# Optimization experiments

Measured on AMD Instinct MI355X. Metric: run time of the kernel, lower is better.

## Reference

```python
import jax, jax.numpy as jnp
import numpy as np

DECAY = 0.99
EPS = 1e-5
COMMIT_COST = 0.25
VQ_COST = 1.0
COUNTER = 1  # first EMA step (hidden buffers are zero-initialized)


def setup_inputs() -> dict:
    key = jax.random.key(0)
    k1, k2 = jax.random.split(key)
    B, D, T, K = 64, 128, 2048, 1024
    x = jax.random.normal(k1, (B, D, T), dtype=jnp.float32)
    # xavier_uniform for [K, D]
    limit = float(np.sqrt(6.0 / (K + D)))
    embeddings = jax.random.uniform(k2, (K, D), minval=-limit, maxval=limit, dtype=jnp.float32)
    ema_dw_hidden = jnp.zeros((K, D), dtype=jnp.float32)
    ema_cluster_hidden = jnp.zeros((K,), dtype=jnp.float32)
    return {"x": x, "embeddings": embeddings,
            "ema_dw_hidden": ema_dw_hidden, "ema_cluster_hidden": ema_cluster_hidden}


def reference(x, embeddings, ema_dw_hidden, ema_cluster_hidden):
    K, D = embeddings.shape
    xt = jnp.transpose(x, (0, 2, 1))          # [B, T, D]
    flat = xt.reshape(-1, D)                  # [N, D]
    dist = (jnp.sum(flat * flat, axis=1, keepdims=True)
            + jnp.sum(embeddings * embeddings, axis=1)
            - 2.0 * flat @ embeddings.T)      # [N, K]
    idx = jnp.argmin(dist, axis=1)            # [N]
    quantized = embeddings[idx].reshape(xt.shape)  # [B, T, D]

    # --- EMA codebook update (no grad; pure stats) ---
    counts = jax.ops.segment_sum(jnp.ones_like(idx, dtype=jnp.float32), idx, num_segments=K)  # [K]
    hid_cs = ema_cluster_hidden - (ema_cluster_hidden - counts) * (1.0 - DECAY)
    avg_cs = hid_cs / (1.0 - DECAY ** COUNTER)
    n = jnp.sum(avg_cs)
    cs = (avg_cs + EPS) / (n + K * EPS) * n   # Laplace-smoothed cluster size
    dw = jax.ops.segment_sum(flat, idx, num_segments=K)  # [K, D] == encodings.T @ flat
    hid_dw = ema_dw_hidden - (ema_dw_hidden - dw) * (1.0 - DECAY)
    avg_dw = hid_dw / (1.0 - DECAY ** COUNTER)
    new_embeddings = avg_dw / cs[:, None]

    # --- losses + straight-through estimator ---
    sg = jax.lax.stop_gradient
    loss_commit = COMMIT_COST * jnp.mean((xt - sg(quantized)) ** 2)
    loss_vq = VQ_COST * jnp.mean((sg(xt) - quantized) ** 2)
    q_st = xt + sg(quantized - xt)
    out = jnp.transpose(q_st, (0, 2, 1))      # [B, D, T]
    return (out, loss_commit, loss_vq, idx, new_embeddings)
```

## Files before the change

### kernel.cpp

```cpp
#include <hip/hip_runtime.h>

#define NB 64
#define ND 128
#define NT 2048
#define NK 1024
#define NN (NB*NT)
#define DTSTRIDE (ND*NT)

typedef __attribute__((ext_vector_type(8))) short bf16x8;
typedef __attribute__((ext_vector_type(4))) float floatx4;

#define WS_ET    0
#define WS_SSX   131072
#define WS_SSE   262144
#define WS_DW    263168
#define WS_CS    394240
#define WS_CNT   395264
#define WS_IDX   396288
#define WS_LOSS  527360
#define WS_OFFS  527364
#define WS_CUR   528388
#define WS_LIST  529412
#define WS_XT    660736
#define WS_EB    17437952

#define O_OUT 0
#define O_LC  16777216
#define O_LV  16777217
#define O_IDX 16777218
#define O_NE  16908290

#define GLL16(g, l) __builtin_amdgcn_global_load_lds( \
    (const __attribute__((address_space(1))) unsigned int*)(g), \
    (__attribute__((address_space(3))) unsigned int*)(l), 16, 0, 0)

__device__ inline void split1(float v, unsigned short &a, unsigned short &b,
                              unsigned short &c) {
    unsigned int u = __float_as_uint(v);
    a = (unsigned short)(u >> 16);
    float f1 = __uint_as_float(u & 0xffff0000u);
    float r = v - f1;
    unsigned int ur = __float_as_uint(r);
    b = (unsigned short)(ur >> 16);
    float f2 = __uint_as_float(ur & 0xffff0000u);
    float r2 = r - f2;
    c = (unsigned short)(__float_as_uint(r2) >> 16);
}

__device__ inline void split2(float va, float vb, unsigned int &p1,
                              unsigned int &p2, unsigned int &p3) {
    unsigned int ua = __float_as_uint(va), ub = __float_as_uint(vb);
    p1 = (ua >> 16) | (ub & 0xffff0000u);
    float fa = __uint_as_float(ua & 0xffff0000u);
    float fb = __uint_as_float(ub & 0xffff0000u);
    float ra = va - fa, rb = vb - fb;
    unsigned int ura = __float_as_uint(ra), urb = __float_as_uint(rb);
    p2 = (ura >> 16) | (urb & 0xffff0000u);
    float f2a = __uint_as_float(ura & 0xffff0000u);
    float f2b = __uint_as_float(urb & 0xffff0000u);
    float r2a = ra - f2a, r2b = rb - f2b;
    p3 = (__float_as_uint(r2a) >> 16) | (__float_as_uint(r2b) & 0xffff0000u);
}

__global__ void prep_e(const float* __restrict__ emb, float* __restrict__ ET,
                       float* __restrict__ sse, unsigned short* __restrict__ eb1,
                       unsigned short* __restrict__ eb2, unsigned short* __restrict__ eb3) {
    int tid = threadIdx.x;
    int k   = blockIdx.x * 16 + (tid >> 4);
    int l   = tid & 15;
    float ss = 0.f;
    #pragma unroll
    for (int it = 0; it < 2; ++it) {
        int d0 = l * 4 + it * 64;
        float4 v = *(const float4*)(emb + k * ND + d0);
        ET[(d0+0)*NK + k] = v.x;
        ET[(d0+1)*NK + k] = v.y;
        ET[(d0+2)*NK + k] = v.z;
        ET[(d0+3)*NK + k] = v.w;
        ss = fmaf(v.x, v.x, ss); ss = fmaf(v.y, v.y, ss);
        ss = fmaf(v.z, v.z, ss); ss = fmaf(v.w, v.w, ss);
        int dc  = (l >> 3) + it * 2;
        int d5  = d0 & 31;
        int qb  = (d5 >> 3) & 3;
        int sl  = qb ^ ((k >> 1) & 3);
        int off = (dc * NK + k) * 32 + (sl << 3) + (d5 & 7);
        ushort4 a, b, c;
        split1(v.x, a.x, b.x, c.x);
        split1(v.y, a.y, b.y, c.y);
        split1(v.z, a.z, b.z, c.z);
        split1(v.w, a.w, b.w, c.w);
        *(ushort4*)(eb1 + off) = a;
        *(ushort4*)(eb2 + off) = b;
        *(ushort4*)(eb3 + off) = c;
    }
    for (int m = 1; m <= 8; m <<= 1) ss += __shfl_xor(ss, m);
    if (l == 0) sse[k] = ss;
}

__global__ void transpose_x(const float* __restrict__ x, float* __restrict__ xt,
                            float* __restrict__ ssx) {
    __shared__ float tile[128][33];
    int tid = threadIdx.x;
    int b   = blockIdx.x >> 6;
    int t0  = (blockIdx.x & 63) << 5;
    int tl  = tid & 31;
    int dg  = tid >> 5;
    const float* xp = x + b * DTSTRIDE + t0 + tl;
    #pragma unroll
    for (int p = 0; p < 16; ++p) {
        int d = p * 8 + dg;
        tile[d][tl] = xp[d * NT];
    }
    __syncthreads();
    float* xtp = xt + (size_t)(b * NT + t0) * ND;
    #pragma unroll
    for (int c = 0; c < 4; ++c) {
        int d = c * 32 + (tid & 31);
        #pragma unroll
        for (int p = 0; p < 4; ++p) {
            int tr = p * 8 + (tid >> 5);
            xtp[tr * ND + d] = tile[d][tr];
        }
    }
    if (tid < 32) {
        float ss = 0.f;
        #pragma unroll 8
        for (int d = 0; d < ND; ++d) {
            float v = tile[d][tid];
            ss = fmaf(v, v, ss);
        }
        ssx[b * NT + t0 + tid] = ss;
    }
}

__device__ __forceinline__ void stage_eb(int ktp, int dcp, int bufidx, int w, int lane,
        unsigned short* smem, const unsigned short* eb1,
        const unsigned short* eb2, const unsigned short* eb3) {
    int goff = (dcp << 15) + (ktp << 12);
    int bufo = bufidx * 12288;
    #pragma unroll
    for (int i = 0; i < 2; ++i) {
        int ch = (w << 1) + i;
        int so = goff + (ch << 9) + (lane << 3);
        GLL16(eb1 + so, &smem[bufo + 0*4096 + (ch << 9)]);
        GLL16(eb2 + so, &smem[bufo + 1*4096 + (ch << 9)]);
        GLL16(eb3 + so, &smem[bufo + 2*4096 + (ch << 9)]);
    }
}

__device__ __forceinline__ int m3(int v) { return v >= 3 ? v - 3 : v; }

__launch_bounds__(256, 2)
__global__ void gemm_argmin_mfma(const float* __restrict__ xt,
                                 const unsigned short* __restrict__ eb1,
                                 const unsigned short* __restrict__ eb2,
                                 const unsigned short* __restrict__ eb3,
                                 const float* __restrict__ ssx, const float* __restrict__ sse,
                                 const float* __restrict__ x, const float* __restrict__ ET,
                                 float* __restrict__ out, int* __restrict__ idxi,
                                 int* __restrict__ counts, float* __restrict__ loss) {
    __shared__ unsigned short smem[38912];
    int tid = threadIdx.x;
    int b   = blockIdx.x >> 4;
    int t0  = (blockIdx.x & 15) << 7;
    int n0  = b * NT + t0;

    int lane = tid & 63;
    int w    = tid >> 6;
    int c    = lane & 15;
    int q    = lane >> 4;
    int slot = q ^ ((c >> 1) & 3);

    stage_eb(0, 0, 0, w, lane, smem, eb1, eb2, eb3);

    float* ssef = (float*)&smem[36864];
    ((float4*)ssef)[tid] = ((const float4*)sse)[tid];

    bf16x8 af[4][2][3];
    #pragma unroll
    for (int dc = 0; dc < 4; ++dc) {
        #pragma unroll
        for (int i = 0; i < 2; ++i) {
            const float* xp = xt + (size_t)(n0 + w*32 + i*16 + c) * ND + dc*32 + q*8;
            float4 v0 = *(const float4*)(xp + 0);
            float4 v1 = *(const float4*)(xp + 4);
            unsigned int p1[4], p2[4], p3[4];
            split2(v0.x, v0.y, p1[0], p2[0], p3[0]);
            split2(v0.z, v0.w, p1[1], p2[1], p3[1]);
            split2(v1.x, v1.y, p1[2], p2[2], p3[2]);
            split2(v1.z, v1.w, p1[3], p2[3], p3[3]);
            uint4 u;
            u = make_uint4(p1[0], p1[1], p1[2], p1[3]); af[dc][i][0] = *(bf16x8*)&u;
            u = make_uint4(p2[0], p2[1], p2[2], p2[3]); af[dc][i][1] = *(bf16x8*)&u;
            u = make_uint4(p3[0], p3[1], p3[2], p3[3]); af[dc][i][2] = *(bf16x8*)&u;
        }
    }

    float ssxv[8];
    #pragma unroll
    for (int i = 0; i < 2; ++i)
        #pragma unroll
        for (int rr = 0; rr < 4; ++rr)
            ssxv[i*4+rr] = ssx[n0 + w*32 + i*16 + q*4 + rr];

    stage_eb(0, 1, 1, w, lane, smem, eb1, eb2, eb3);

    float bestD[8]; int bestK[8];
    #pragma unroll
    for (int i = 0; i < 8; ++i) { bestD[i] = 3.4e38f; bestK[i] = 0; }

    floatx4 acc[2][8];
    int b3 = 0;

    for (int kt = 0; kt < 8; ++kt) {
        #pragma unroll
        for (int i = 0; i < 2; ++i)
            #pragma unroll
            for (int j = 0; j < 8; ++j)
                acc[i][j] = (floatx4){0.f, 0.f, 0.f, 0.f};

        #pragma unroll
        for (int dc = 0; dc < 4; ++dc) {
            int cur = (dc == 0 || dc == 3) ? b3 : m3(b3 + dc);

            if (kt == 7 && dc == 3) {
                asm volatile("s_waitcnt vmcnt(0) lgkmcnt(0)" ::: "memory");
            } else {
                asm volatile("s_waitcnt vmcnt(6) lgkmcnt(0)" ::: "memory");
            }
            __builtin_amdgcn_s_barrier();

            if (dc == 0) {
                stage_eb(kt, 2, m3(b3 + 2), w, lane, smem, eb1, eb2, eb3);
            } else if (dc == 1) {
                stage_eb(kt, 3, b3, w, lane, smem, eb1, eb2, eb3);
            } else if (dc == 2) {
                if (kt < 7) stage_eb(kt + 1, 0, m3(b3 + 1), w, lane, smem, eb1, eb2, eb3);
            } else {
                if (kt < 7) stage_eb(kt + 1, 1, m3(b3 + 2), w, lane, smem, eb1, eb2, eb3);
            }

            int bufo = cur * 12288;
            __builtin_amdgcn_s_setprio(1);
            #pragma unroll
            for (int j = 0; j < 8; ++j) {
                int ro = bufo + ((j << 4) + c) * 32 + slot * 8;
                bf16x8 b1 = *(const bf16x8*)(&smem[ro + 0*4096]);
                bf16x8 b2 = *(const bf16x8*)(&smem[ro + 1*4096]);
                bf16x8 b3f = *(const bf16x8*)(&smem[ro + 2*4096]);
                #pragma unroll
                for (int i = 0; i < 2; ++i) {
                    acc[i][j] = __builtin_amdgcn_mfma_f32_16x16x32_bf16(af[dc][i][0], b1, acc[i][j], 0, 0, 0);
                    acc[i][j] = __builtin_amdgcn_mfma_f32_16x16x32_bf16(af[dc][i][0], b2, acc[i][j], 0, 0, 0);
                    acc[i][j] = __builtin_amdgcn_mfma_f32_16x16x32_bf16(af[dc][i][1], b1, acc[i][j], 0, 0, 0);
                    acc[i][j] = __builtin_amdgcn_mfma_f32_16x16x32_bf16(af[dc][i][1], b2, acc[i][j], 0, 0, 0);
                    acc[i][j] = __builtin_amdgcn_mfma_f32_16x16x32_bf16(af[dc][i][0], b3f, acc[i][j], 0, 0, 0);
                    acc[i][j] = __builtin_amdgcn_mfma_f32_16x16x32_bf16(af[dc][i][2], b1, acc[i][j], 0, 0, 0);
                }
            }
            __builtin_amdgcn_s_setprio(0);
        }

        #pragma unroll
        for (int j = 0; j < 8; ++j) {
            int   kidx = (kt << 7) + (j << 4) + c;
            float se = ssef[(kt << 7) + (j << 4) + c];
            #pragma unroll
            for (int i = 0; i < 2; ++i) {
                #pragma unroll
                for (int rr = 0; rr < 4; ++rr) {
                    float t1   = ssxv[i*4+rr] + se;
                    float dist = fmaf(-2.f, acc[i][j][rr], t1);
                    if (dist < bestD[i*4+rr]) { bestD[i*4+rr] = dist; bestK[i*4+rr] = kidx; }
                }
            }
        }
        b3 = m3(b3 + 1);
    }

    #pragma unroll
    for (int i = 0; i < 8; ++i) {
        float d = bestD[i]; int kk = bestK[i];
        for (int m = 1; m <= 8; m <<= 1) {
            float od = __shfl_xor(d, m);
            int   ok = __shfl_xor(kk, m);
            if (od < d || (od == d && ok < kk)) { d = od; kk = ok; }
        }
        bestD[i] = d; bestK[i] = kk;
    }
    int* ksh = (int*)smem;
    if (c == 0) {
        float ls = 0.f;
        #pragma unroll
        for (int i = 0; i < 2; ++i)
            #pragma unroll
            for (int rr = 0; rr < 4; ++rr) {
                int r  = w*32 + i*16 + q*4 + rr;
                int n  = n0 + r;
                int kk = bestK[i*4+rr];
                out[O_IDX + n] = (float)kk;
                idxi[n] = kk;
                ksh[r] = kk;
                atomicAdd(&counts[kk], 1);
                ls += bestD[i*4+rr];
            }
        atomicAdd(loss, ls);
    }
    __syncthreads();

    int tl2 = tid & 127;
    int dh  = tid >> 7;
    int kk2 = ksh[tl2];
    const float* xp2 = x + b * DTSTRIDE + t0 + tl2;
    float*       op2 = out + O_OUT + b * DTSTRIDE + t0 + tl2;
    #pragma unroll 4
    for (int s = 0; s < 64; ++s) {
        int d = s * 2 + dh;
        float xv = xp2[d * NT];
        float qv = ET[d * NK + kk2];
        op2[d * NT] = xv + (qv - xv);
    }
}

__global__ void scan_cs(const int* __restrict__ counts, int* __restrict__ offs,
                        int* __restrict__ cur, const float* __restrict__ ch,
                        const float* __restrict__ loss, float* __restrict__ csv,
                        float* __restrict__ out) {
    __shared__ int   s[256];
    __shared__ float red[256];
    int tid = threadIdx.x;
    int c[4]; int sum = 0;
    #pragma unroll
    for (int j = 0; j < 4; ++j) { c[j] = counts[tid*4+j]; sum += c[j]; }
    s[tid] = sum; __syncthreads();
    for (int off = 1; off < 256; off <<= 1) {
        int v = (tid >= off) ? s[tid - off] : 0;
        __syncthreads();
        s[tid] += v;
        __syncthreads();
    }
    int base = (tid == 0) ? 0 : s[tid-1];
    #pragma unroll
    for (int j = 0; j < 4; ++j) {
        offs[tid*4+j] = base; cur[tid*4+j] = base; base += c[j];
    }
    __syncthreads();
    const float DECF = (float)(1.0 - 0.99);
    float sf = 0.f;
    #pragma unroll
    for (int rr = 0; rr < 4; ++rr) {
        int k = tid + rr * 256;
        float cc = (float)counts[k];
        float e = ch[k];
        float hid = e - (e - cc) * DECF;
        sf += hid / DECF;
    }
    red[tid] = sf; __syncthreads();
    for (int off = 128; off > 0; off >>= 1) {
        if (tid < off) red[tid] += red[tid + off];
        __syncthreads();
    }
    float n = red[0];
    const float KEPSF = (float)(1024.0 * 1e-5);
    #pragma unroll
    for (int rr = 0; rr < 4; ++rr) {
        int k = tid + rr * 256;
        float cc = (float)counts[k];
        float e = ch[k];
        float hid = e - (e - cc) * DECF;
        float a = hid / DECF;
        csv[k] = (a + 1e-5f) / (n + KEPSF) * n;
    }
    if (tid == 0) {
        float mean = loss[0] / 16777216.f;
        out[O_LC] = 0.25f * mean;
        out[O_LV] = mean;
    }
}

__global__ void fill_list(const int* __restrict__ idxi, int* __restrict__ cur,
                          int* __restrict__ list) {
    int n = blockIdx.x * 256 + threadIdx.x;
    int k = idxi[n];
    int pos = atomicAdd(&cur[k], 1);
    list[pos] = n;
}

__global__ void dw_sum(const float* __restrict__ xt,
                       const int* __restrict__ counts, const int* __restrict__ offs,
                       const int* __restrict__ list, const float* __restrict__ dwh,
                       const float* __restrict__ csv, float* __restrict__ out) {
    __shared__ float red[128];
    int k = blockIdx.x;
    int d = threadIdx.x & 127;
    int h = threadIdx.x >> 7;
    int cnt = counts[k], base = offs[k];
    float acc = 0.f;
    for (int m = h; m < cnt; m += 2) {
        int n = list[base + m];
        acc += xt[(size_t)n * ND + d];
    }
    if (h == 1) red[d] = acc;
    __syncthreads();
    if (h == 0) {
        const float DECF = (float)(1.0 - 0.99);
        float dwv = acc + red[d];
        int   kd  = k * ND + d;
        float e   = dwh[kd];
        float hid = e - (e - dwv) * DECF;
        float a   = hid / DECF;
        out[O_NE + kd] = a / csv[k];
    }
}

extern "C" void kernel_launch(void* const* d_in, const int* in_sizes, int n_in,
                              void* d_out, int out_size, void* d_ws, size_t ws_size,
                              hipStream_t stream) {
    const float* x   = (const float*)d_in[0];
    const float* emb = (const float*)d_in[1];
    const float* dwh = (const float*)d_in[2];
    const float* ch  = (const float*)d_in[3];
    float* out = (float*)d_out;
    float* ws  = (float*)d_ws;

    float* ET   = ws + WS_ET;
    float* ssx  = ws + WS_SSX;
    float* sse  = ws + WS_SSE;
    float* csv  = ws + WS_CS;
    int*   counts = (int*)(ws + WS_CNT);
    int*   idxi   = (int*)(ws + WS_IDX);
    float* loss   = ws + WS_LOSS;
    int*   offs   = (int*)(ws + WS_OFFS);
    int*   cur    = (int*)(ws + WS_CUR);
    int*   list   = (int*)(ws + WS_LIST);
    float* xt     = ws + WS_XT;
    unsigned short* eb1 = (unsigned short*)(ws + WS_EB);
    unsigned short* eb2 = eb1 + NK * ND;
    unsigned short* eb3 = eb2 + NK * ND;

    hipMemsetAsync(counts, 0, NK * sizeof(int), stream);
    hipMemsetAsync(loss, 0, sizeof(float), stream);

    prep_e         <<<64,   256, 0, stream>>>(emb, ET, sse, eb1, eb2, eb3);
    transpose_x    <<<4096, 256, 0, stream>>>(x, xt, ssx);
    gemm_argmin_mfma<<<1024,256, 0, stream>>>(xt, eb1, eb2, eb3, ssx, sse, x, ET,
                                              out, idxi, counts, loss);
    scan_cs        <<<1,    256, 0, stream>>>(counts, offs, cur, ch, loss, csv, out);
    fill_list      <<<512,  256, 0, stream>>>(idxi, cur, list);
    dw_sum         <<<1024, 256, 0, stream>>>(xt, counts, offs, list, dwh, csv, out);
}
```

Measured before the change: 424.4 us.

## Fuse x transpose and row-norm computation into the GEMM-argmin kernel

Removes the separate transpose_x kernel. The GEMM kernel now loads its 128-token tile of x directly in [D,T] layout, transposes it through shared memory, builds the split-bf16 A fragments and row squared norms from it, and still writes xt for the later dw_sum kernel. This cuts one launch and the extra global read of xt by the GEMM. In exchange it adds shared-memory staging with extra barriers, and the eb staging now starts after the x prologue instead of overlapping with it.

```diff
diff --git a/kernel.cpp b/kernel.cpp
--- a/kernel.cpp
+++ b/kernel.cpp
@@ -97,42 +97,6 @@
     if (l == 0) sse[k] = ss;
 }
 
-__global__ void transpose_x(const float* __restrict__ x, float* __restrict__ xt,
-                            float* __restrict__ ssx) {
-    __shared__ float tile[128][33];
-    int tid = threadIdx.x;
-    int b   = blockIdx.x >> 6;
-    int t0  = (blockIdx.x & 63) << 5;
-    int tl  = tid & 31;
-    int dg  = tid >> 5;
-    const float* xp = x + b * DTSTRIDE + t0 + tl;
-    #pragma unroll
-    for (int p = 0; p < 16; ++p) {
-        int d = p * 8 + dg;
-        tile[d][tl] = xp[d * NT];
-    }
-    __syncthreads();
-    float* xtp = xt + (size_t)(b * NT + t0) * ND;
-    #pragma unroll
-    for (int c = 0; c < 4; ++c) {
-        int d = c * 32 + (tid & 31);
-        #pragma unroll
-        for (int p = 0; p < 4; ++p) {
-            int tr = p * 8 + (tid >> 5);
-            xtp[tr * ND + d] = tile[d][tr];
-        }
-    }
-    if (tid < 32) {
-        float ss = 0.f;
-        #pragma unroll 8
-        for (int d = 0; d < ND; ++d) {
-            float v = tile[d][tid];
-            ss = fmaf(v, v, ss);
-        }
-        ssx[b * NT + t0 + tid] = ss;
-    }
-}
-
 __device__ __forceinline__ void stage_eb(int ktp, int dcp, int bufidx, int w, int lane,
         unsigned short* smem, const unsigned short* eb1,
         const unsigned short* eb2, const unsigned short* eb3) {
@@ -151,11 +115,11 @@
 __device__ __forceinline__ int m3(int v) { return v >= 3 ? v - 3 : v; }
 
 __launch_bounds__(256, 2)
-__global__ void gemm_argmin_mfma(const float* __restrict__ xt,
+__global__ void gemm_argmin_mfma(float* __restrict__ xt,
                                  const unsigned short* __restrict__ eb1,
                                  const unsigned short* __restrict__ eb2,
                                  const unsigned short* __restrict__ eb3,
-                                 const float* __restrict__ ssx, const float* __restrict__ sse,
+                                 const float* __restrict__ sse,
                                  const float* __restrict__ x, const float* __restrict__ ET,
                                  float* __restrict__ out, int* __restrict__ idxi,
                                  int* __restrict__ counts, float* __restrict__ loss) {
@@ -171,38 +135,79 @@
     int q    = lane >> 4;
     int slot = q ^ ((c >> 1) & 3);
 
-    stage_eb(0, 0, 0, w, lane, smem, eb1, eb2, eb3);
-
-    float* ssef = (float*)&smem[36864];
-    ((float4*)ssef)[tid] = ((const float4*)sse)[tid];
-
+    float* ax   = (float*)(smem + 24576);
+    float* ssxr = (float*)(smem + 32832);
+    float* ssef = (float*)(smem + 36864);
+
+    float4 ssetmp = ((const float4*)sse)[tid];
+
+    const float* xbase = x + (size_t)b * DTSTRIDE + t0;
     bf16x8 af[4][2][3];
+    float ssacc = 0.f;
     #pragma unroll
     for (int dc = 0; dc < 4; ++dc) {
+        float4 cv[4];
+        #pragma unroll
+        for (int rep = 0; rep < 4; ++rep) {
+            int d  = rep * 8 + (tid >> 5);
+            int t4 = (tid & 31) * 4;
+            cv[rep] = *(const float4*)(xbase + (size_t)(dc*32 + d) * NT + t4);
+        }
+        __syncthreads();
+        #pragma unroll
+        for (int rep = 0; rep < 4; ++rep) {
+            int d  = rep * 8 + (tid >> 5);
+            int t4 = (tid & 31) * 4;
+            *(float4*)(ax + d * 129 + t4) = cv[rep];
+        }
+        __syncthreads();
         #pragma unroll
         for (int i = 0; i < 2; ++i) {
-            const float* xp = xt + (size_t)(n0 + w*32 + i*16 + c) * ND + dc*32 + q*8;
-            float4 v0 = *(const float4*)(xp + 0);
-            float4 v1 = *(const float4*)(xp + 4);
+            int r = w*32 + i*16 + c;
+            float v[8];
+            #pragma unroll
+            for (int j = 0; j < 8; ++j) v[j] = ax[(q*8 + j) * 129 + r];
             unsigned int p1[4], p2[4], p3[4];
-            split2(v0.x, v0.y, p1[0], p2[0], p3[0]);
-            split2(v0.z, v0.w, p1[1], p2[1], p3[1]);
-            split2(v1.x, v1.y, p1[2], p2[2], p3[2]);
-            split2(v1.z, v1.w, p1[3], p2[3], p3[3]);
+            split2(v[0], v[1], p1[0], p2[0], p3[0]);
+            split2(v[2], v[3], p1[1], p2[1], p3[1]);
+            split2(v[4], v[5], p1[2], p2[2], p3[2]);
+            split2(v[6], v[7], p1[3], p2[3], p3[3]);
             uint4 u;
             u = make_uint4(p1[0], p1[1], p1[2], p1[3]); af[dc][i][0] = *(bf16x8*)&u;
             u = make_uint4(p2[0], p2[1], p2[2], p2[3]); af[dc][i][1] = *(bf16x8*)&u;
             u = make_uint4(p3[0], p3[1], p3[2], p3[3]); af[dc][i][2] = *(bf16x8*)&u;
         }
-    }
+        if (tid < 128) {
+            #pragma unroll 8
+            for (int d5 = 0; d5 < 32; ++d5) {
+                float v = ax[d5 * 129 + tid];
+                ssacc = fmaf(v, v, ssacc);
+            }
+        }
+        {
+            int tl = tid & 127, dh = tid >> 7;
+            #pragma unroll
+            for (int rep = 0; rep < 4; ++rep) {
+                int d = dh * 16 + rep * 4;
+                float4 vv;
+                vv.x = ax[(d+0)*129 + tl]; vv.y = ax[(d+1)*129 + tl];
+                vv.z = ax[(d+2)*129 + tl]; vv.w = ax[(d+3)*129 + tl];
+                *(float4*)(xt + (size_t)(n0 + tl) * ND + dc*32 + d) = vv;
+            }
+        }
+    }
+    if (tid < 128) ssxr[tid] = ssacc;
+    ((float4*)ssef)[tid] = ssetmp;
+    __syncthreads();
 
     float ssxv[8];
     #pragma unroll
     for (int i = 0; i < 2; ++i)
         #pragma unroll
         for (int rr = 0; rr < 4; ++rr)
-            ssxv[i*4+rr] = ssx[n0 + w*32 + i*16 + q*4 + rr];
-
+            ssxv[i*4+rr] = ssxr[w*32 + i*16 + q*4 + rr];
+
+    stage_eb(0, 0, 0, w, lane, smem, eb1, eb2, eb3);
     stage_eb(0, 1, 1, w, lane, smem, eb1, eb2, eb3);
 
     float bestD[8]; int bestK[8];
@@ -424,7 +429,6 @@
     float* ws  = (float*)d_ws;
 
     float* ET   = ws + WS_ET;
-    float* ssx  = ws + WS_SSX;
     float* sse  = ws + WS_SSE;
     float* csv  = ws + WS_CS;
     int*   counts = (int*)(ws + WS_CNT);
@@ -442,8 +446,7 @@
     hipMemsetAsync(loss, 0, sizeof(float), stream);
 
     prep_e         <<<64,   256, 0, stream>>>(emb, ET, sse, eb1, eb2, eb3);
-    transpose_x    <<<4096, 256, 0, stream>>>(x, xt, ssx);
-    gemm_argmin_mfma<<<1024,256, 0, stream>>>(xt, eb1, eb2, eb3, ssx, sse, x, ET,
+    gemm_argmin_mfma<<<1024,256, 0, stream>>>(xt, eb1, eb2, eb3, sse, x, ET,
                                               out, idxi, counts, loss);
     scan_cs        <<<1,    256, 0, stream>>>(counts, offs, cur, ch, loss, csv, out);
     fill_list      <<<512,  256, 0, stream>>>(idxi, cur, list);
```

Measured after the change: 433.6 us. 1.02x slower.
